# Kernel tuning notes

Hardware: AMD Instinct MI355X
Metric: run time of the kernel (lower is better)

## Reference

```python
import jax, jax.numpy as jnp
import numpy as np

WBITS_MAX = 3.0   # 3-bit signed narrow-range weights: levels in [-3, 3]
ABITS_MAX = 15.0  # 4-bit unsigned activations: levels in [0, 15]


def round_ste(x):
    # straight-through estimator for round (Brevitas uses STE)
    return x + jax.lax.stop_gradient(jnp.round(x) - x)


def quant_weight(w):
    # per-tensor symmetric narrow-range 3-bit fake quant (Int weight per-tensor float)
    s = jnp.max(jnp.abs(w)) / WBITS_MAX
    wq = jnp.clip(round_ste(w / s), -WBITS_MAX, WBITS_MAX) * s
    return wq, s


def quant_bias(b, w_scale, in_step):
    # Brevitas BiasQuant: bias scale = input_scale * weight_scale, no clipping (wide int)
    sb = w_scale * in_step  # in_step is shape (1,)
    return round_ste(b / sb) * sb


def quant_relu(x, s):
    # QuantReLU(bit_width=4): relu then unsigned 4-bit fake quant with learned scale s
    step = s / ABITS_MAX
    return jnp.clip(round_ste(jax.nn.relu(x) / step), 0.0, ABITS_MAX) * step


def conv2d(x, w):
    return jax.lax.conv_general_dilated(
        x, w, window_strides=(1, 1), padding='VALID',
        dimension_numbers=('NCHW', 'OIHW', 'NCHW'))


def maxpool2(x):
    return jax.lax.reduce_window(x, -jnp.inf, jax.lax.max,
                                 (1, 1, 2, 2), (1, 1, 2, 2), 'VALID')


def setup_inputs() -> dict:
    key = jax.random.key(0)
    ks = jax.random.split(key, 16)
    d = {}
    d['x'] = jax.random.normal(ks[0], (256, 3, 160, 160), jnp.float32)
    d['w1'] = jax.random.normal(ks[1], (6, 3, 3, 3), jnp.float32) * 0.2
    d['w2'] = jax.random.normal(ks[2], (12, 6, 3, 3), jnp.float32) * 0.2
    d['b2'] = jax.random.normal(ks[3], (12,), jnp.float32) * 0.1
    d['w3'] = jax.random.normal(ks[4], (18, 12, 3, 3), jnp.float32) * 0.2
    d['b3'] = jax.random.normal(ks[5], (18,), jnp.float32) * 0.1
    d['w4'] = jax.random.normal(ks[6], (18, 18, 3, 3), jnp.float32) * 0.2
    d['b4'] = jax.random.normal(ks[7], (18,), jnp.float32) * 0.1
    d['w5'] = jax.random.normal(ks[8], (18, 18, 3, 3), jnp.float32) * 0.2
    d['b5'] = jax.random.normal(ks[9], (18,), jnp.float32) * 0.1
    d['fw1'] = jax.random.normal(ks[10], (120, 162), jnp.float32) * 0.1
    d['fb1'] = jax.random.normal(ks[11], (120,), jnp.float32) * 0.1
    d['fw2'] = jax.random.normal(ks[12], (84, 120), jnp.float32) * 0.1
    d['fb2'] = jax.random.normal(ks[13], (84,), jnp.float32) * 0.1
    d['fw3'] = jax.random.normal(ks[14], (9, 84), jnp.float32) * 0.1
    for i in range(1, 8):
        d[f's{i}'] = jnp.full((1,), 6.0, jnp.float32)  # learned act scales (calibrated init)
    return d


def reference(x, w1, w2, b2, w3, b3, w4, b4, w5, b5,
              fw1, fb1, fw2, fb2, fw3, s1, s2, s3, s4, s5, s6, s7):
    # stage 1 (note: original forward feeds raw x into conv1, bypassing quant_inp)
    q1, _ = quant_weight(w1)
    out = maxpool2(quant_relu(conv2d(x, q1), s1))            # [B,6,79,79]
    # stage 2
    q2, ws2 = quant_weight(w2)
    bq2 = quant_bias(b2, ws2, s1 / ABITS_MAX)
    out = maxpool2(quant_relu(conv2d(out, q2) + bq2[None, :, None, None], s2))  # [B,12,38,38]
    # stage 3
    q3, ws3 = quant_weight(w3)
    bq3 = quant_bias(b3, ws3, s2 / ABITS_MAX)
    out = maxpool2(quant_relu(conv2d(out, q3) + bq3[None, :, None, None], s3))  # [B,18,18,18]
    # stage 4
    q4, ws4 = quant_weight(w4)
    bq4 = quant_bias(b4, ws4, s3 / ABITS_MAX)
    out = maxpool2(quant_relu(conv2d(out, q4) + bq4[None, :, None, None], s4))  # [B,18,8,8]
    # stage 5
    q5, ws5 = quant_weight(w5)
    bq5 = quant_bias(b5, ws5, s4 / ABITS_MAX)
    out = maxpool2(quant_relu(conv2d(out, q5) + bq5[None, :, None, None], s5))  # [B,18,3,3]
    out = out.reshape(out.shape[0], -1)                      # [B,162]
    # fc1
    qf1, fs1 = quant_weight(fw1)
    bqf1 = quant_bias(fb1, fs1, s5 / ABITS_MAX)
    out = quant_relu(out @ qf1.T + bqf1, s6)                 # [B,120]
    # fc2
    qf2, fs2 = quant_weight(fw2)
    bqf2 = quant_bias(fb2, fs2, s6 / ABITS_MAX)
    out = quant_relu(out @ qf2.T + bqf2, s7)                 # [B,84]
    # fc3 (no bias, output not re-quantized: return_quant_tensor=False default path)
    qf3, _ = quant_weight(fw3)
    return out @ qf3.T                                       # [B,9]
```

## Files before the change

### kernel.cpp

```cpp
#include <hip/hip_runtime.h>
#include <hip/hip_bf16.h>
#include <math.h>

constexpr size_t OFF_OUT1 = 0;
constexpr size_t OFF_OUT2 = (size_t)256 * 6 * 79 * 80;

template<int CIN, int COUT, int NCO, int HIN, int WSIN,
         int HPOOL, int WPOOL, int WSOUT, int XG, int RB,
         int THREADS, bool HAS_BIAS>
__global__ __launch_bounds__(THREADS)
void conv_stage(const float* __restrict__ in,
                const float* __restrict__ w_raw,
                const float* __restrict__ b_raw,
                const float* __restrict__ s_prev,
                const float* __restrict__ s_act,
                float* __restrict__ out)
{
    constexpr int GROUPS = COUT / NCO;
    constexpr int W4IN   = WSIN / 4;
    constexpr int NW     = COUT * CIN * 9;
    constexpr int STEPS  = 4 * CIN;
    static_assert(NCO * GROUPS == COUT, "NCO divides COUT");
    static_assert(GROUPS * XG * RB <= THREADS, "single compute pass");
    static_assert(4 * XG == WSOUT, "full padded row coverage");
    static_assert(WSIN % 4 == 0, "vec4 loads");

    __shared__ float lw[NW];
    __shared__ float lb[COUT];
    __shared__ float red[THREADS];

    const int r0  = blockIdx.x * RB;
    const int n   = blockIdx.y;
    const int tid = threadIdx.x;

    float mx = 0.0f;
    for (int i = tid; i < NW; i += THREADS) {
        const float v = w_raw[i];
        lw[i] = v;
        mx = fmaxf(mx, fabsf(v));
    }
    if (HAS_BIAS)
        for (int i = tid; i < COUT; i += THREADS) lb[i] = b_raw[i];
    red[tid] = mx;
    __syncthreads();
    for (int s = THREADS / 2; s > 0; s >>= 1) {
        if (tid < s) red[tid] = fmaxf(red[tid], red[tid + s]);
        __syncthreads();
    }
    const float sw_ = red[0] / 3.0f;
    for (int i = tid; i < NW; i += THREADS) {
        float q = rintf(lw[i] / sw_);
        q = fminf(fmaxf(q, -3.0f), 3.0f);
        lw[i] = q * sw_;
    }
    if (HAS_BIAS) {
        const float sb = sw_ * (s_prev[0] / 15.0f);
        for (int i = tid; i < COUT; i += THREADS)
            lb[i] = rintf(lb[i] / sb) * sb;
    }
    __syncthreads();

    const int o = tid;
    if (o >= GROUPS * XG * RB) return;
    const int cog = o % GROUPS;
    const int xg  = (o / GROUPS) % XG;
    const int ry  = o / (GROUPS * XG);
    const int r   = r0 + ry;
    if (r >= HPOOL) return;

    const float step = s_act[0] / 15.0f;

    const int u0 = 2 * xg;
    const int u1 = 2 * xg + 1;
    const int u2 = (2 * xg + 2 < W4IN) ? (2 * xg + 2) : (W4IN - 1);

    const float* base = in + (size_t)n * CIN * HIN * WSIN + (size_t)(2 * r) * WSIN;

    float acc[NCO][16];
#pragma unroll
    for (int j = 0; j < NCO; ++j)
#pragma unroll
        for (int i = 0; i < 16; ++i) acc[j][i] = 0.0f;

    float4 buf[3][3];
    float  wv[NCO][9];

#define ISSUE_STEP(S)                                                          \
    {                                                                          \
        const float* rp = base + (size_t)((S) >> 2) * HIN * WSIN               \
                               + (size_t)((S) & 3) * WSIN;                     \
        buf[(S) % 3][0] = *(const float4*)&rp[4 * u0];                         \
        buf[(S) % 3][1] = *(const float4*)&rp[4 * u1];                         \
        buf[(S) % 3][2] = *(const float4*)&rp[4 * u2];                         \
    }

    ISSUE_STEP(0);
    ISSUE_STEP(1);

#pragma unroll
    for (int s = 0; s < STEPS; ++s) {
        const int c  = s >> 2;
        const int rr = s & 3;

        if (s + 2 < STEPS) ISSUE_STEP(s + 2);

        if (rr == 0) {
#pragma unroll
            for (int j = 0; j < NCO; ++j)
#pragma unroll
                for (int k = 0; k < 9; ++k)
                    wv[j][k] = lw[((NCO * cog + j) * CIN + c) * 9 + k];
        }

        const float* row = (const float*)buf[s % 3];

        if (rr < 3) {
#pragma unroll
            for (int j = 0; j < NCO; ++j)
#pragma unroll
                for (int kc = 0; kc < 3; ++kc)
#pragma unroll
                    for (int xx = 0; xx < 8; ++xx)
                        acc[j][xx] = fmaf(row[xx + kc], wv[j][rr * 3 + kc], acc[j][xx]);
        }
        if (rr >= 1) {
#pragma unroll
            for (int j = 0; j < NCO; ++j)
#pragma unroll
                for (int kc = 0; kc < 3; ++kc)
#pragma unroll
                    for (int xx = 0; xx < 8; ++xx)
                        acc[j][8 + xx] = fmaf(row[xx + kc], wv[j][(rr - 1) * 3 + kc], acc[j][8 + xx]);
        }
    }
#undef ISSUE_STEP

#pragma unroll
    for (int j = 0; j < NCO; ++j) {
        const int co = NCO * cog + j;
        const float bias = HAS_BIAS ? lb[co] : 0.0f;
        float4 st;
#pragma unroll
        for (int t = 0; t < 4; ++t) {
            float m = fmaxf(fmaxf(acc[j][2 * t], acc[j][2 * t + 1]),
                            fmaxf(acc[j][8 + 2 * t], acc[j][8 + 2 * t + 1]));
            float v = fmaxf(m + bias, 0.0f);
            float q = rintf(v / step);
            q = fminf(fmaxf(q, 0.0f), 15.0f);
            ((float*)&st)[t] = (4 * xg + t < WPOOL) ? q * step : 0.0f;
        }
        *(float4*)&out[(((size_t)n * COUT + co) * HPOOL + r) * WSOUT + 4 * xg] = st;
    }
}

__global__ __launch_bounds__(512)
void tail_mega(const float* __restrict__ in2,
               const float* __restrict__ w3, const float* __restrict__ b3,
               const float* __restrict__ w4, const float* __restrict__ b4,
               const float* __restrict__ w5, const float* __restrict__ b5,
               const float* __restrict__ fw1, const float* __restrict__ fb1,
               const float* __restrict__ fw2, const float* __restrict__ fb2,
               const float* __restrict__ fw3,
               const float* __restrict__ s2, const float* __restrict__ s3,
               const float* __restrict__ s4, const float* __restrict__ s5,
               const float* __restrict__ s6, const float* __restrict__ s7,
               float* __restrict__ out)
{
    __shared__ float SL[12 * 38 * 40];
    __shared__ float A3[18 * 18 * 18];
    __shared__ float W3q[1944], W4q[2916], W5q[2916];
    __shared__ float B3q[18], B4q[18], B5q[18];
    __shared__ float O4[18 * 8 * 8];
    __shared__ float A5[162], A6[120], A7[84];

    const int n   = blockIdx.x;
    const int tid = threadIdx.x;
    float* red = A3;

    {
        const float4* src = (const float4*)(in2 + (size_t)n * 18240);
        float4* dst = (float4*)SL;
        for (int i = tid; i < 4560; i += 512) dst[i] = src[i];
    }
    float m3 = 0.f, m4 = 0.f, m5 = 0.f, g1 = 0.f, g2 = 0.f, g3 = 0.f;
    for (int i = tid; i < 1944; i += 512) { const float v = w3[i]; W3q[i] = v; m3 = fmaxf(m3, fabsf(v)); }
    for (int i = tid; i < 2916; i += 512) { const float v = w4[i]; W4q[i] = v; m4 = fmaxf(m4, fabsf(v)); }
    for (int i = tid; i < 2916; i += 512) { const float v = w5[i]; W5q[i] = v; m5 = fmaxf(m5, fabsf(v)); }
    for (int i = tid; i < 19440; i += 512) g1 = fmaxf(g1, fabsf(fw1[i]));
    for (int i = tid; i < 10080; i += 512) g2 = fmaxf(g2, fabsf(fw2[i]));
    for (int i = tid; i <   756; i += 512) g3 = fmaxf(g3, fabsf(fw3[i]));
    if (tid < 18) { B3q[tid] = b3[tid]; B4q[tid] = b4[tid]; B5q[tid] = b5[tid]; }
    red[0 * 512 + tid] = m3; red[1 * 512 + tid] = m4; red[2 * 512 + tid] = m5;
    red[3 * 512 + tid] = g1; red[4 * 512 + tid] = g2; red[5 * 512 + tid] = g3;
    __syncthreads();
    for (int s = 256; s > 0; s >>= 1) {
        if (tid < s)
#pragma unroll
            for (int j = 0; j < 6; ++j)
                red[j * 512 + tid] = fmaxf(red[j * 512 + tid], red[j * 512 + tid + s]);
        __syncthreads();
    }
    const float sw3 = red[0] / 3.0f, sw4 = red[512] / 3.0f, sw5 = red[1024] / 3.0f;
    const float sf1 = red[1536] / 3.0f, sf2 = red[2048] / 3.0f, sf3 = red[2560] / 3.0f;

    for (int i = tid; i < 1944; i += 512) { float q = rintf(W3q[i] / sw3); q = fminf(fmaxf(q, -3.f), 3.f); W3q[i] = q * sw3; }
    for (int i = tid; i < 2916; i += 512) { float q = rintf(W4q[i] / sw4); q = fminf(fmaxf(q, -3.f), 3.f); W4q[i] = q * sw4; }
    for (int i = tid; i < 2916; i += 512) { float q = rintf(W5q[i] / sw5); q = fminf(fmaxf(q, -3.f), 3.f); W5q[i] = q * sw5; }
    if (tid < 18) {
        const float sb3 = sw3 * (s2[0] / 15.0f); B3q[tid] = rintf(B3q[tid] / sb3) * sb3;
        const float sb4 = sw4 * (s3[0] / 15.0f); B4q[tid] = rintf(B4q[tid] / sb4) * sb4;
        const float sb5 = sw5 * (s4[0] / 15.0f); B5q[tid] = rintf(B5q[tid] / sb5) * sb5;
    }
    __syncthreads();

    {
        const float st = s3[0] / 15.0f;
        for (int it = tid; it < 972; it += 512) {
            const int r  = it / 54;
            const int rm = it - r * 54;
            const int co = rm / 3;
            const int th = rm - co * 3;

            float acc0[12], acc1[12];
#pragma unroll
            for (int i = 0; i < 12; ++i) { acc0[i] = 0.f; acc1[i] = 0.f; }

            for (int c = 0; c < 12; ++c) {
                float wv[9];
#pragma unroll
                for (int k = 0; k < 9; ++k) wv[k] = W3q[(co * 12 + c) * 9 + k];
#pragma unroll
                for (int rr = 0; rr < 4; ++rr) {
                    const float* rp = &SL[(c * 38 + 2 * r + rr) * 40 + 12 * th];
                    float row[14];
#pragma unroll
                    for (int v = 0; v < 7; ++v)
                        *(float2*)&row[2 * v] = *(const float2*)&rp[2 * v];
                    if (rr < 3) {
#pragma unroll
                        for (int kc = 0; kc < 3; ++kc)
#pragma unroll
                            for (int xx = 0; xx < 12; ++xx)
                                acc0[xx] = fmaf(row[xx + kc], wv[rr * 3 + kc], acc0[xx]);
                    }
                    if (rr >= 1) {
#pragma unroll
                        for (int kc = 0; kc < 3; ++kc)
#pragma unroll
                            for (int xx = 0; xx < 12; ++xx)
                                acc1[xx] = fmaf(row[xx + kc], wv[(rr - 1) * 3 + kc], acc1[xx]);
                    }
                }
            }
            const float bias = B3q[co];
#pragma unroll
            for (int x = 0; x < 6; ++x) {
                float m = fmaxf(fmaxf(acc0[2 * x], acc0[2 * x + 1]),
                                fmaxf(acc1[2 * x], acc1[2 * x + 1]));
                float v = fmaxf(m + bias, 0.0f);
                float q = rintf(v / st);
                q = fminf(fmaxf(q, 0.0f), 15.0f);
                A3[(co * 18 + r) * 18 + 6 * th + x] = q * st;
            }
        }
    }
    __syncthreads();

    {
        const float st = s4[0] / 15.0f;
        for (int o = tid; o < 1152; o += 512) {
            const int co = o >> 6;
            const int r  = (o >> 3) & 7;
            const int x  = o & 7;
            float a00 = 0.f, a01 = 0.f, a10 = 0.f, a11 = 0.f;
            for (int c = 0; c < 18; ++c) {
                float win[4][4];
#pragma unroll
                for (int rr = 0; rr < 4; ++rr) {
                    const int base = (c * 18 + 2 * r + rr) * 18 + 2 * x;
                    *(float2*)&win[rr][0] = *(const float2*)&A3[base];
                    *(float2*)&win[rr][2] = *(const float2*)&A3[base + 2];
                }
                const float* wp = &W4q[(co * 18 + c) * 9];
#pragma unroll
                for (int kr = 0; kr < 3; ++kr)
#pragma unroll
                    for (int kc = 0; kc < 3; ++kc) {
                        const float wv = wp[kr * 3 + kc];
                        a00 = fmaf(win[kr    ][kc    ], wv, a00);
                        a01 = fmaf(win[kr    ][kc + 1], wv, a01);
                        a10 = fmaf(win[kr + 1][kc    ], wv, a10);
                        a11 = fmaf(win[kr + 1][kc + 1], wv, a11);
                    }
            }
            float m = fmaxf(fmaxf(a00, a01), fmaxf(a10, a11));
            float v = fmaxf(m + B4q[co], 0.0f);
            float q = rintf(v / st);
            q = fminf(fmaxf(q, 0.0f), 15.0f);
            O4[o] = q * st;
        }
    }
    __syncthreads();

    {
        const float st = s5[0] / 15.0f;
        if (tid < 162) {
            const int co  = tid / 9;
            const int rem = tid - co * 9;
            const int r   = rem / 3;
            const int x   = rem - r * 3;
            float a00 = 0.f, a01 = 0.f, a10 = 0.f, a11 = 0.f;
            for (int c = 0; c < 18; ++c) {
                float win[4][4];
#pragma unroll
                for (int rr = 0; rr < 4; ++rr) {
                    const int base = c * 64 + (2 * r + rr) * 8 + 2 * x;
                    *(float2*)&win[rr][0] = *(const float2*)&O4[base];
                    *(float2*)&win[rr][2] = *(const float2*)&O4[base + 2];
                }
                const float* wp = &W5q[(co * 18 + c) * 9];
#pragma unroll
                for (int kr = 0; kr < 3; ++kr)
#pragma unroll
                    for (int kc = 0; kc < 3; ++kc) {
                        const float wv = wp[kr * 3 + kc];
                        a00 = fmaf(win[kr    ][kc    ], wv, a00);
                        a01 = fmaf(win[kr    ][kc + 1], wv, a01);
                        a10 = fmaf(win[kr + 1][kc    ], wv, a10);
                        a11 = fmaf(win[kr + 1][kc + 1], wv, a11);
                    }
            }
            float m = fmaxf(fmaxf(a00, a01), fmaxf(a10, a11));
            float v = fmaxf(m + B5q[co], 0.0f);
            float q = rintf(v / st);
            q = fminf(fmaxf(q, 0.0f), 15.0f);
            A5[tid] = q * st;
        }
    }
    __syncthreads();

    if (tid < 120) {
        float acc = 0.f;
        const float* wr = fw1 + (size_t)tid * 162;
#pragma unroll 6
        for (int k = 0; k < 162; ++k) {
            float q = rintf(wr[k] / sf1);
            q = fminf(fmaxf(q, -3.f), 3.f);
            acc = fmaf(A5[k], q * sf1, acc);
        }
        const float sb = sf1 * (s5[0] / 15.0f);
        acc += rintf(fb1[tid] / sb) * sb;
        const float st = s6[0] / 15.0f;
        float q = rintf(fmaxf(acc, 0.0f) / st);
        q = fminf(fmaxf(q, 0.0f), 15.0f);
        A6[tid] = q * st;
    }
    __syncthreads();

    if (tid < 84) {
        float acc = 0.f;
        const float* wr = fw2 + (size_t)tid * 120;
#pragma unroll 6
        for (int k = 0; k < 120; ++k) {
            float q = rintf(wr[k] / sf2);
            q = fminf(fmaxf(q, -3.f), 3.f);
            acc = fmaf(A6[k], q * sf2, acc);
        }
        const float sb = sf2 * (s6[0] / 15.0f);
        acc += rintf(fb2[tid] / sb) * sb;
        const float st = s7[0] / 15.0f;
        float q = rintf(fmaxf(acc, 0.0f) / st);
        q = fminf(fmaxf(q, 0.0f), 15.0f);
        A7[tid] = q * st;
    }
    __syncthreads();

    if (tid < 9) {
        float acc = 0.f;
        const float* wr = fw3 + (size_t)tid * 84;
#pragma unroll 6
        for (int k = 0; k < 84; ++k) {
            float q = rintf(wr[k] / sf3);
            q = fminf(fmaxf(q, -3.f), 3.f);
            acc = fmaf(A7[k], q * sf3, acc);
        }
        out[(size_t)n * 9 + tid] = acc;
    }
}

extern "C" void kernel_launch(void* const* d_in, const int* in_sizes, int n_in,
                              void* d_out, int out_size, void* d_ws, size_t ws_size,
                              hipStream_t stream)
{
    const float* x   = (const float*)d_in[0];
    const float* w1  = (const float*)d_in[1];
    const float* w2  = (const float*)d_in[2];
    const float* b2  = (const float*)d_in[3];
    const float* w3  = (const float*)d_in[4];
    const float* b3  = (const float*)d_in[5];
    const float* w4  = (const float*)d_in[6];
    const float* b4  = (const float*)d_in[7];
    const float* w5  = (const float*)d_in[8];
    const float* b5  = (const float*)d_in[9];
    const float* fw1 = (const float*)d_in[10];
    const float* fb1 = (const float*)d_in[11];
    const float* fw2 = (const float*)d_in[12];
    const float* fb2 = (const float*)d_in[13];
    const float* fw3 = (const float*)d_in[14];
    const float* s1  = (const float*)d_in[15];
    const float* s2  = (const float*)d_in[16];
    const float* s3  = (const float*)d_in[17];
    const float* s4  = (const float*)d_in[18];
    const float* s5  = (const float*)d_in[19];
    const float* s6  = (const float*)d_in[20];
    const float* s7  = (const float*)d_in[21];

    float* ws = (float*)d_ws;
    float* out = (float*)d_out;

    conv_stage<3, 6, 2, 160, 160, 79, 79, 80, 20, 4, 256, false>
        <<<dim3(20, 256), 256, 0, stream>>>(x, w1, nullptr, nullptr, s1, ws + OFF_OUT1);

    conv_stage<6, 12, 2, 79, 80, 38, 38, 40, 10, 4, 256, true>
        <<<dim3(10, 256), 256, 0, stream>>>(ws + OFF_OUT1, w2, b2, s1, s2, ws + OFF_OUT2);

    tail_mega<<<256, 512, 0, stream>>>(ws + OFF_OUT2,
                                       w3, b3, w4, b4, w5, b5,
                                       fw1, fb1, fw2, fb2, fw3,
                                       s2, s3, s4, s5, s6, s7, out);
}
```

Baseline: 152.8 us.

## Split conv3 out of tail megakernel into its own two-block-per-image stage

```diff
diff --git a/kernel.cpp b/kernel.cpp
--- a/kernel.cpp
+++ b/kernel.cpp
@@ -4,6 +4,7 @@
 
 constexpr size_t OFF_OUT1 = 0;
 constexpr size_t OFF_OUT2 = (size_t)256 * 6 * 79 * 80;
+constexpr size_t OFF_A3   = OFF_OUT1;
 
 template<int CIN, int COUT, int NCO, int HIN, int WSIN,
          int HPOOL, int WPOOL, int WSOUT, int XG, int RB,
@@ -154,115 +155,166 @@
 }
 
 __global__ __launch_bounds__(512)
-void tail_mega(const float* __restrict__ in2,
-               const float* __restrict__ w3, const float* __restrict__ b3,
-               const float* __restrict__ w4, const float* __restrict__ b4,
-               const float* __restrict__ w5, const float* __restrict__ b5,
-               const float* __restrict__ fw1, const float* __restrict__ fb1,
-               const float* __restrict__ fw2, const float* __restrict__ fb2,
-               const float* __restrict__ fw3,
-               const float* __restrict__ s2, const float* __restrict__ s3,
-               const float* __restrict__ s4, const float* __restrict__ s5,
-               const float* __restrict__ s6, const float* __restrict__ s7,
-               float* __restrict__ out)
+void conv3_stage(const float* __restrict__ in2,
+                 const float* __restrict__ w3, const float* __restrict__ b3,
+                 const float* __restrict__ s2, const float* __restrict__ s3,
+                 float* __restrict__ a3)
 {
-    __shared__ float SL[12 * 38 * 40];
-    __shared__ float A3[18 * 18 * 18];
-    __shared__ float W3q[1944], W4q[2916], W5q[2916];
-    __shared__ float B3q[18], B4q[18], B5q[18];
-    __shared__ float O4[18 * 8 * 8];
+    __shared__ float lw[1944];
+    __shared__ float lb[18];
+    __shared__ float red[512];
+
+    const int rb  = blockIdx.x;
+    const int n   = blockIdx.y;
+    const int tid = threadIdx.x;
+
+    float mx = 0.0f;
+    for (int i = tid; i < 1944; i += 512) {
+        const float v = w3[i];
+        lw[i] = v;
+        mx = fmaxf(mx, fabsf(v));
+    }
+    if (tid < 18) lb[tid] = b3[tid];
+    red[tid] = mx;
+    __syncthreads();
+    for (int s = 256; s > 0; s >>= 1) {
+        if (tid < s) red[tid] = fmaxf(red[tid], red[tid + s]);
+        __syncthreads();
+    }
+    const float sw = red[0] / 3.0f;
+    for (int i = tid; i < 1944; i += 512) {
+        float q = rintf(lw[i] / sw);
+        q = fminf(fmaxf(q, -3.0f), 3.0f);
+        lw[i] = q * sw;
+    }
+    if (tid < 18) {
+        const float sb = sw * (s2[0] / 15.0f);
+        lb[tid] = rintf(lb[tid] / sb) * sb;
+    }
+    __syncthreads();
+
+    if (tid >= 486) return;
+    const int rloc = tid / 54;
+    const int rm   = tid - rloc * 54;
+    const int co   = rm / 3;
+    const int th   = rm - co * 3;
+    const int r    = rb * 9 + rloc;
+
+    const float st = s3[0] / 15.0f;
+    const float* base = in2 + (size_t)n * 18240 + (size_t)(2 * r) * 40 + 12 * th;
+
+    float acc0[12], acc1[12];
+#pragma unroll
+    for (int i = 0; i < 12; ++i) { acc0[i] = 0.f; acc1[i] = 0.f; }
+
+    for (int c = 0; c < 12; ++c) {
+        float wv[9];
+#pragma unroll
+        for (int k = 0; k < 9; ++k) wv[k] = lw[(co * 12 + c) * 9 + k];
+        const float* cp = base + (size_t)c * 1520;
+#pragma unroll
+        for (int rr = 0; rr < 4; ++rr) {
+            const float* rp = cp + rr * 40;
+            float row[14];
+#pragma unroll
+            for (int v = 0; v < 7; ++v)
+                *(float2*)&row[2 * v] = *(const float2*)&rp[2 * v];
+            if (rr < 3) {
+#pragma unroll
+                for (int kc = 0; kc < 3; ++kc)
+#pragma unroll
+                    for (int xx = 0; xx < 12; ++xx)
+                        acc0[xx] = fmaf(row[xx + kc], wv[rr * 3 + kc], acc0[xx]);
+            }
+            if (rr >= 1) {
+#pragma unroll
+                for (int kc = 0; kc < 3; ++kc)
+#pragma unroll
+                    for (int xx = 0; xx < 12; ++xx)
+                        acc1[xx] = fmaf(row[xx + kc], wv[(rr - 1) * 3 + kc], acc1[xx]);
+            }
+        }
+    }
+
+    const float bias = lb[co];
+    float* orow = a3 + (size_t)n * 5832 + (size_t)co * 324 + (size_t)r * 18 + 6 * th;
+#pragma unroll
+    for (int x = 0; x < 6; ++x) {
+        float m = fmaxf(fmaxf(acc0[2 * x], acc0[2 * x + 1]),
+                        fmaxf(acc1[2 * x], acc1[2 * x + 1]));
+        float v = fmaxf(m + bias, 0.0f);
+        float q = rintf(v / st);
+        q = fminf(fmaxf(q, 0.0f), 15.0f);
+        orow[x] = q * st;
+    }
+}
+
+__global__ __launch_bounds__(512)
+void tail456(const float* __restrict__ a3in,
+             const float* __restrict__ w4, const float* __restrict__ b4,
+             const float* __restrict__ w5, const float* __restrict__ b5,
+             const float* __restrict__ fw1, const float* __restrict__ fb1,
+             const float* __restrict__ fw2, const float* __restrict__ fb2,
+             const float* __restrict__ fw3,
+             const float* __restrict__ s3, const float* __restrict__ s4,
+             const float* __restrict__ s5, const float* __restrict__ s6,
+             const float* __restrict__ s7,
+             float* __restrict__ out)
+{
+    __shared__ float A3[5832];
+    __shared__ float W4q[2916], W5q[2916];
+    __shared__ float B4q[18], B5q[18];
+    __shared__ float O4[1152];
     __shared__ float A5[162], A6[120], A7[84];
+    __shared__ float red[5 * 512];
 
     const int n   = blockIdx.x;
     const int tid = threadIdx.x;
-    float* red = A3;
 
     {
-        const float4* src = (const float4*)(in2 + (size_t)n * 18240);
-        float4* dst = (float4*)SL;
-        for (int i = tid; i < 4560; i += 512) dst[i] = src[i];
-    }
-    float m3 = 0.f, m4 = 0.f, m5 = 0.f, g1 = 0.f, g2 = 0.f, g3 = 0.f;
-    for (int i = tid; i < 1944; i += 512) { const float v = w3[i]; W3q[i] = v; m3 = fmaxf(m3, fabsf(v)); }
+        const float4* src = (const float4*)(a3in + (size_t)n * 5832);
+        float4* dst = (float4*)A3;
+        for (int i = tid; i < 1458; i += 512) dst[i] = src[i];
+    }
+    float m4 = 0.f, m5 = 0.f, g1 = 0.f, g2 = 0.f, g3 = 0.f;
     for (int i = tid; i < 2916; i += 512) { const float v = w4[i]; W4q[i] = v; m4 = fmaxf(m4, fabsf(v)); }
     for (int i = tid; i < 2916; i += 512) { const float v = w5[i]; W5q[i] = v; m5 = fmaxf(m5, fabsf(v)); }
-    for (int i = tid; i < 19440; i += 512) g1 = fmaxf(g1, fabsf(fw1[i]));
-    for (int i = tid; i < 10080; i += 512) g2 = fmaxf(g2, fabsf(fw2[i]));
-    for (int i = tid; i <   756; i += 512) g3 = fmaxf(g3, fabsf(fw3[i]));
-    if (tid < 18) { B3q[tid] = b3[tid]; B4q[tid] = b4[tid]; B5q[tid] = b5[tid]; }
-    red[0 * 512 + tid] = m3; red[1 * 512 + tid] = m4; red[2 * 512 + tid] = m5;
-    red[3 * 512 + tid] = g1; red[4 * 512 + tid] = g2; red[5 * 512 + tid] = g3;
+    {
+        const float4* f1 = (const float4*)fw1;
+        for (int i = tid; i < 4860; i += 512) {
+            const float4 v = f1[i];
+            g1 = fmaxf(g1, fmaxf(fmaxf(fabsf(v.x), fabsf(v.y)), fmaxf(fabsf(v.z), fabsf(v.w))));
+        }
+        const float4* f2 = (const float4*)fw2;
+        for (int i = tid; i < 2520; i += 512) {
+            const float4 v = f2[i];
+            g2 = fmaxf(g2, fmaxf(fmaxf(fabsf(v.x), fabsf(v.y)), fmaxf(fabsf(v.z), fabsf(v.w))));
+        }
+        const float4* f3 = (const float4*)fw3;
+        for (int i = tid; i < 189; i += 512) {
+            const float4 v = f3[i];
+            g3 = fmaxf(g3, fmaxf(fmaxf(fabsf(v.x), fabsf(v.y)), fmaxf(fabsf(v.z), fabsf(v.w))));
+        }
+    }
+    if (tid < 18) { B4q[tid] = b4[tid]; B5q[tid] = b5[tid]; }
+    red[tid] = m4; red[512 + tid] = m5; red[1024 + tid] = g1;
+    red[1536 + tid] = g2; red[2048 + tid] = g3;
     __syncthreads();
     for (int s = 256; s > 0; s >>= 1) {
         if (tid < s)
 #pragma unroll
-            for (int j = 0; j < 6; ++j)
+            for (int j = 0; j < 5; ++j)
                 red[j * 512 + tid] = fmaxf(red[j * 512 + tid], red[j * 512 + tid + s]);
         __syncthreads();
     }
-    const float sw3 = red[0] / 3.0f, sw4 = red[512] / 3.0f, sw5 = red[1024] / 3.0f;
-    const float sf1 = red[1536] / 3.0f, sf2 = red[2048] / 3.0f, sf3 = red[2560] / 3.0f;
-
-    for (int i = tid; i < 1944; i += 512) { float q = rintf(W3q[i] / sw3); q = fminf(fmaxf(q, -3.f), 3.f); W3q[i] = q * sw3; }
+    const float sw4 = red[0] / 3.0f, sw5 = red[512] / 3.0f;
+    const float sf1 = red[1024] / 3.0f, sf2 = red[1536] / 3.0f, sf3 = red[2048] / 3.0f;
+
     for (int i = tid; i < 2916; i += 512) { float q = rintf(W4q[i] / sw4); q = fminf(fmaxf(q, -3.f), 3.f); W4q[i] = q * sw4; }
     for (int i = tid; i < 2916; i += 512) { float q = rintf(W5q[i] / sw5); q = fminf(fmaxf(q, -3.f), 3.f); W5q[i] = q * sw5; }
     if (tid < 18) {
-        const float sb3 = sw3 * (s2[0] / 15.0f); B3q[tid] = rintf(B3q[tid] / sb3) * sb3;
         const float sb4 = sw4 * (s3[0] / 15.0f); B4q[tid] = rintf(B4q[tid] / sb4) * sb4;
         const float sb5 = sw5 * (s4[0] / 15.0f); B5q[tid] = rintf(B5q[tid] / sb5) * sb5;
-    }
-    __syncthreads();
-
-    {
-        const float st = s3[0] / 15.0f;
-        for (int it = tid; it < 972; it += 512) {
-            const int r  = it / 54;
-            const int rm = it - r * 54;
-            const int co = rm / 3;
-            const int th = rm - co * 3;
-
-            float acc0[12], acc1[12];
-#pragma unroll
-            for (int i = 0; i < 12; ++i) { acc0[i] = 0.f; acc1[i] = 0.f; }
-
-            for (int c = 0; c < 12; ++c) {
-                float wv[9];
-#pragma unroll
-                for (int k = 0; k < 9; ++k) wv[k] = W3q[(co * 12 + c) * 9 + k];
-#pragma unroll
-                for (int rr = 0; rr < 4; ++rr) {
-                    const float* rp = &SL[(c * 38 + 2 * r + rr) * 40 + 12 * th];
-                    float row[14];
-#pragma unroll
-                    for (int v = 0; v < 7; ++v)
-                        *(float2*)&row[2 * v] = *(const float2*)&rp[2 * v];
-                    if (rr < 3) {
-#pragma unroll
-                        for (int kc = 0; kc < 3; ++kc)
-#pragma unroll
-                            for (int xx = 0; xx < 12; ++xx)
-                                acc0[xx] = fmaf(row[xx + kc], wv[rr * 3 + kc], acc0[xx]);
-                    }
-                    if (rr >= 1) {
-#pragma unroll
-                        for (int kc = 0; kc < 3; ++kc)
-#pragma unroll
-                            for (int xx = 0; xx < 12; ++xx)
-                                acc1[xx] = fmaf(row[xx + kc], wv[(rr - 1) * 3 + kc], acc1[xx]);
-                    }
-                }
-            }
-            const float bias = B3q[co];
-#pragma unroll
-            for (int x = 0; x < 6; ++x) {
-                float m = fmaxf(fmaxf(acc0[2 * x], acc0[2 * x + 1]),
-                                fmaxf(acc1[2 * x], acc1[2 * x + 1]));
-                float v = fmaxf(m + bias, 0.0f);
-                float q = rintf(v / st);
-                q = fminf(fmaxf(q, 0.0f), 15.0f);
-                A3[(co * 18 + r) * 18 + 6 * th + x] = q * st;
-            }
-        }
     }
     __syncthreads();
 
@@ -277,7 +329,7 @@
                 float win[4][4];
 #pragma unroll
                 for (int rr = 0; rr < 4; ++rr) {
-                    const int base = (c * 18 + 2 * r + rr) * 18 + 2 * x;
+                    const int base = c * 324 + (2 * r + rr) * 18 + 2 * x;
                     *(float2*)&win[rr][0] = *(const float2*)&A3[base];
                     *(float2*)&win[rr][2] = *(const float2*)&A3[base + 2];
                 }
@@ -424,8 +476,10 @@
     conv_stage<6, 12, 2, 79, 80, 38, 38, 40, 10, 4, 256, true>
         <<<dim3(10, 256), 256, 0, stream>>>(ws + OFF_OUT1, w2, b2, s1, s2, ws + OFF_OUT2);
 
-    tail_mega<<<256, 512, 0, stream>>>(ws + OFF_OUT2,
-                                       w3, b3, w4, b4, w5, b5,
-                                       fw1, fb1, fw2, fb2, fw3,
-                                       s2, s3, s4, s5, s6, s7, out);
+    conv3_stage<<<dim3(2, 256), 512, 0, stream>>>(ws + OFF_OUT2, w3, b3, s2, s3, ws + OFF_A3);
+
+    tail456<<<256, 512, 0, stream>>>(ws + OFF_A3,
+                                     w4, b4, w5, b5,
+                                     fw1, fb1, fw2, fb2, fw3,
+                                     s3, s4, s5, s6, s7, out);
 }
```

Result: slower. 162.6 us (+6.4%).

## Store intermediate activations as uint8 quant levels and widen tail kernel

Applied to the files above, without the earlier changes.

```diff
diff --git a/kernel.cpp b/kernel.cpp
--- a/kernel.cpp
+++ b/kernel.cpp
@@ -1,21 +1,23 @@
 #include <hip/hip_runtime.h>
 #include <hip/hip_bf16.h>
 #include <math.h>
-
-constexpr size_t OFF_OUT1 = 0;
-constexpr size_t OFF_OUT2 = (size_t)256 * 6 * 79 * 80;
+#include <type_traits>
+
+constexpr size_t OFF_OUT1B = 0;
+constexpr size_t OFF_OUT2B = (size_t)256 * 6 * 79 * 80;
 
 template<int CIN, int COUT, int NCO, int HIN, int WSIN,
          int HPOOL, int WPOOL, int WSOUT, int XG, int RB,
-         int THREADS, bool HAS_BIAS>
+         int THREADS, bool HAS_BIAS, bool IN_U8>
 __global__ __launch_bounds__(THREADS)
-void conv_stage(const float* __restrict__ in,
+void conv_stage(const void* __restrict__ in_,
                 const float* __restrict__ w_raw,
                 const float* __restrict__ b_raw,
                 const float* __restrict__ s_prev,
                 const float* __restrict__ s_act,
-                float* __restrict__ out)
+                unsigned char* __restrict__ out)
 {
+    using TIN = typename std::conditional<IN_U8, unsigned char, float>::type;
     constexpr int GROUPS = COUT / NCO;
     constexpr int W4IN   = WSIN / 4;
     constexpr int NW     = COUT * CIN * 9;
@@ -69,12 +71,15 @@
     if (r >= HPOOL) return;
 
     const float step = s_act[0] / 15.0f;
+    float step_in = 0.0f;
+    if constexpr (IN_U8) step_in = s_prev[0] / 15.0f;
 
     const int u0 = 2 * xg;
     const int u1 = 2 * xg + 1;
     const int u2 = (2 * xg + 2 < W4IN) ? (2 * xg + 2) : (W4IN - 1);
 
-    const float* base = in + (size_t)n * CIN * HIN * WSIN + (size_t)(2 * r) * WSIN;
+    const TIN* in   = (const TIN*)in_;
+    const TIN* base = in + (size_t)n * CIN * HIN * WSIN + (size_t)(2 * r) * WSIN;
 
     float acc[NCO][16];
 #pragma unroll
@@ -82,16 +87,23 @@
 #pragma unroll
         for (int i = 0; i < 16; ++i) acc[j][i] = 0.0f;
 
-    float4 buf[3][3];
-    float  wv[NCO][9];
+    float4       fbuf[3][3];
+    unsigned int ubuf[3][3];
+    float        wv[NCO][9];
 
 #define ISSUE_STEP(S)                                                          \
     {                                                                          \
-        const float* rp = base + (size_t)((S) >> 2) * HIN * WSIN               \
-                               + (size_t)((S) & 3) * WSIN;                     \
-        buf[(S) % 3][0] = *(const float4*)&rp[4 * u0];                         \
-        buf[(S) % 3][1] = *(const float4*)&rp[4 * u1];                         \
-        buf[(S) % 3][2] = *(const float4*)&rp[4 * u2];                         \
+        const TIN* rp = base + (size_t)((S) >> 2) * HIN * WSIN                 \
+                             + (size_t)((S) & 3) * WSIN;                       \
+        if constexpr (IN_U8) {                                                 \
+            ubuf[(S) % 3][0] = *(const unsigned int*)&rp[4 * u0];              \
+            ubuf[(S) % 3][1] = *(const unsigned int*)&rp[4 * u1];              \
+            ubuf[(S) % 3][2] = *(const unsigned int*)&rp[4 * u2];              \
+        } else {                                                               \
+            fbuf[(S) % 3][0] = *(const float4*)&rp[4 * u0];                    \
+            fbuf[(S) % 3][1] = *(const float4*)&rp[4 * u1];                    \
+            fbuf[(S) % 3][2] = *(const float4*)&rp[4 * u2];                    \
+        }                                                                      \
     }
 
     ISSUE_STEP(0);
@@ -112,7 +124,20 @@
                     wv[j][k] = lw[((NCO * cog + j) * CIN + c) * 9 + k];
         }
 
-        const float* row = (const float*)buf[s % 3];
+        float row[12];
+        if constexpr (IN_U8) {
+#pragma unroll
+            for (int k = 0; k < 3; ++k) {
+                const unsigned int d = ubuf[s % 3][k];
+#pragma unroll
+                for (int b = 0; b < 4; ++b)
+                    row[4 * k + b] = (float)((d >> (8 * b)) & 0xffu) * step_in;
+            }
+        } else {
+            const float* rv = (const float*)fbuf[s % 3];
+#pragma unroll
+            for (int i = 0; i < 12; ++i) row[i] = rv[i];
+        }
 
         if (rr < 3) {
 #pragma unroll
@@ -139,7 +164,7 @@
     for (int j = 0; j < NCO; ++j) {
         const int co = NCO * cog + j;
         const float bias = HAS_BIAS ? lb[co] : 0.0f;
-        float4 st;
+        unsigned int pck = 0;
 #pragma unroll
         for (int t = 0; t < 4; ++t) {
             float m = fmaxf(fmaxf(acc[j][2 * t], acc[j][2 * t + 1]),
@@ -147,14 +172,22 @@
             float v = fmaxf(m + bias, 0.0f);
             float q = rintf(v / step);
             q = fminf(fmaxf(q, 0.0f), 15.0f);
-            ((float*)&st)[t] = (4 * xg + t < WPOOL) ? q * step : 0.0f;
-        }
-        *(float4*)&out[(((size_t)n * COUT + co) * HPOOL + r) * WSOUT + 4 * xg] = st;
+            const unsigned int qi = (4 * xg + t < WPOOL) ? (unsigned int)q : 0u;
+            pck |= qi << (8 * t);
+        }
+        *(unsigned int*)&out[(((size_t)n * COUT + co) * HPOOL + r) * WSOUT + 4 * xg] = pck;
     }
 }
 
-__global__ __launch_bounds__(512)
-void tail_mega(const float* __restrict__ in2,
+__device__ __forceinline__ float wave_max(float v) {
+#pragma unroll
+    for (int off = 32; off > 0; off >>= 1)
+        v = fmaxf(v, __shfl_down(v, off));
+    return v;
+}
+
+__global__ __launch_bounds__(1024)
+void tail_mega(const unsigned char* __restrict__ in2,
                const float* __restrict__ w3, const float* __restrict__ b3,
                const float* __restrict__ w4, const float* __restrict__ b4,
                const float* __restrict__ w5, const float* __restrict__ b5,
@@ -166,46 +199,67 @@
                const float* __restrict__ s6, const float* __restrict__ s7,
                float* __restrict__ out)
 {
-    __shared__ float SL[12 * 38 * 40];
-    __shared__ float A3[18 * 18 * 18];
+    __shared__ unsigned int SLu[4560];
+    __shared__ float A3[5832];
     __shared__ float W3q[1944], W4q[2916], W5q[2916];
     __shared__ float B3q[18], B4q[18], B5q[18];
-    __shared__ float O4[18 * 8 * 8];
+    __shared__ float O4[1152];
     __shared__ float A5[162], A6[120], A7[84];
-
-    const int n   = blockIdx.x;
-    const int tid = threadIdx.x;
-    float* red = A3;
+    __shared__ float sm[16][6];
+    __shared__ float scales[6];
+
+    const int n    = blockIdx.x;
+    const int tid  = threadIdx.x;
+    const int wid  = tid >> 6;
+    const int lane = tid & 63;
 
     {
-        const float4* src = (const float4*)(in2 + (size_t)n * 18240);
-        float4* dst = (float4*)SL;
-        for (int i = tid; i < 4560; i += 512) dst[i] = src[i];
+        const uint4* src = (const uint4*)(in2 + (size_t)n * 18240);
+        uint4* dst = (uint4*)SLu;
+        for (int i = tid; i < 1140; i += 1024) dst[i] = src[i];
     }
     float m3 = 0.f, m4 = 0.f, m5 = 0.f, g1 = 0.f, g2 = 0.f, g3 = 0.f;
-    for (int i = tid; i < 1944; i += 512) { const float v = w3[i]; W3q[i] = v; m3 = fmaxf(m3, fabsf(v)); }
-    for (int i = tid; i < 2916; i += 512) { const float v = w4[i]; W4q[i] = v; m4 = fmaxf(m4, fabsf(v)); }
-    for (int i = tid; i < 2916; i += 512) { const float v = w5[i]; W5q[i] = v; m5 = fmaxf(m5, fabsf(v)); }
-    for (int i = tid; i < 19440; i += 512) g1 = fmaxf(g1, fabsf(fw1[i]));
-    for (int i = tid; i < 10080; i += 512) g2 = fmaxf(g2, fabsf(fw2[i]));
-    for (int i = tid; i <   756; i += 512) g3 = fmaxf(g3, fabsf(fw3[i]));
+    for (int i = tid; i < 1944; i += 1024) { const float v = w3[i]; W3q[i] = v; m3 = fmaxf(m3, fabsf(v)); }
+    for (int i = tid; i < 2916; i += 1024) { const float v = w4[i]; W4q[i] = v; m4 = fmaxf(m4, fabsf(v)); }
+    for (int i = tid; i < 2916; i += 1024) { const float v = w5[i]; W5q[i] = v; m5 = fmaxf(m5, fabsf(v)); }
+    {
+        const float4* f1 = (const float4*)fw1;
+        for (int i = tid; i < 4860; i += 1024) {
+            const float4 v = f1[i];
+            g1 = fmaxf(g1, fmaxf(fmaxf(fabsf(v.x), fabsf(v.y)), fmaxf(fabsf(v.z), fabsf(v.w))));
+        }
+        const float4* f2 = (const float4*)fw2;
+        for (int i = tid; i < 2520; i += 1024) {
+            const float4 v = f2[i];
+            g2 = fmaxf(g2, fmaxf(fmaxf(fabsf(v.x), fabsf(v.y)), fmaxf(fabsf(v.z), fabsf(v.w))));
+        }
+        const float4* f3 = (const float4*)fw3;
+        for (int i = tid; i < 189; i += 1024) {
+            const float4 v = f3[i];
+            g3 = fmaxf(g3, fmaxf(fmaxf(fabsf(v.x), fabsf(v.y)), fmaxf(fabsf(v.z), fabsf(v.w))));
+        }
+    }
     if (tid < 18) { B3q[tid] = b3[tid]; B4q[tid] = b4[tid]; B5q[tid] = b5[tid]; }
-    red[0 * 512 + tid] = m3; red[1 * 512 + tid] = m4; red[2 * 512 + tid] = m5;
-    red[3 * 512 + tid] = g1; red[4 * 512 + tid] = g2; red[5 * 512 + tid] = g3;
-    __syncthreads();
-    for (int s = 256; s > 0; s >>= 1) {
-        if (tid < s)
-#pragma unroll
-            for (int j = 0; j < 6; ++j)
-                red[j * 512 + tid] = fmaxf(red[j * 512 + tid], red[j * 512 + tid + s]);
-        __syncthreads();
-    }
-    const float sw3 = red[0] / 3.0f, sw4 = red[512] / 3.0f, sw5 = red[1024] / 3.0f;
-    const float sf1 = red[1536] / 3.0f, sf2 = red[2048] / 3.0f, sf3 = red[2560] / 3.0f;
-
-    for (int i = tid; i < 1944; i += 512) { float q = rintf(W3q[i] / sw3); q = fminf(fmaxf(q, -3.f), 3.f); W3q[i] = q * sw3; }
-    for (int i = tid; i < 2916; i += 512) { float q = rintf(W4q[i] / sw4); q = fminf(fmaxf(q, -3.f), 3.f); W4q[i] = q * sw4; }
-    for (int i = tid; i < 2916; i += 512) { float q = rintf(W5q[i] / sw5); q = fminf(fmaxf(q, -3.f), 3.f); W5q[i] = q * sw5; }
+    m3 = wave_max(m3); m4 = wave_max(m4); m5 = wave_max(m5);
+    g1 = wave_max(g1); g2 = wave_max(g2); g3 = wave_max(g3);
+    if (lane == 0) {
+        sm[wid][0] = m3; sm[wid][1] = m4; sm[wid][2] = m5;
+        sm[wid][3] = g1; sm[wid][4] = g2; sm[wid][5] = g3;
+    }
+    __syncthreads();
+    if (tid < 6) {
+        float v = sm[0][tid];
+#pragma unroll
+        for (int w = 1; w < 16; ++w) v = fmaxf(v, sm[w][tid]);
+        scales[tid] = v / 3.0f;
+    }
+    __syncthreads();
+    const float sw3 = scales[0], sw4 = scales[1], sw5 = scales[2];
+    const float sf1 = scales[3], sf2 = scales[4], sf3 = scales[5];
+
+    for (int i = tid; i < 1944; i += 1024) { float q = rintf(W3q[i] / sw3); q = fminf(fmaxf(q, -3.f), 3.f); W3q[i] = q * sw3; }
+    for (int i = tid; i < 2916; i += 1024) { float q = rintf(W4q[i] / sw4); q = fminf(fmaxf(q, -3.f), 3.f); W4q[i] = q * sw4; }
+    for (int i = tid; i < 2916; i += 1024) { float q = rintf(W5q[i] / sw5); q = fminf(fmaxf(q, -3.f), 3.f); W5q[i] = q * sw5; }
     if (tid < 18) {
         const float sb3 = sw3 * (s2[0] / 15.0f); B3q[tid] = rintf(B3q[tid] / sb3) * sb3;
         const float sb4 = sw4 * (s3[0] / 15.0f); B4q[tid] = rintf(B4q[tid] / sb4) * sb4;
@@ -214,10 +268,12 @@
     __syncthreads();
 
     {
+        const unsigned char* SLb = (const unsigned char*)SLu;
+        const float step2 = s2[0] / 15.0f;
         const float st = s3[0] / 15.0f;
-        for (int it = tid; it < 972; it += 512) {
-            const int r  = it / 54;
-            const int rm = it - r * 54;
+        if (tid < 972) {
+            const int r  = tid / 54;
+            const int rm = tid - r * 54;
             const int co = rm / 3;
             const int th = rm - co * 3;
 
@@ -226,29 +282,33 @@
             for (int i = 0; i < 12; ++i) { acc0[i] = 0.f; acc1[i] = 0.f; }
 
             for (int c = 0; c < 12; ++c) {
-                float wv[9];
-#pragma unroll
-                for (int k = 0; k < 9; ++k) wv[k] = W3q[(co * 12 + c) * 9 + k];
+                float wvv[9];
+#pragma unroll
+                for (int k = 0; k < 9; ++k) wvv[k] = W3q[(co * 12 + c) * 9 + k];
 #pragma unroll
                 for (int rr = 0; rr < 4; ++rr) {
-                    const float* rp = &SL[(c * 38 + 2 * r + rr) * 40 + 12 * th];
-                    float row[14];
-#pragma unroll
-                    for (int v = 0; v < 7; ++v)
-                        *(float2*)&row[2 * v] = *(const float2*)&rp[2 * v];
+                    const int off = (c * 38 + 2 * r + rr) * 40 + 12 * th;
+                    float row[16];
+#pragma unroll
+                    for (int k = 0; k < 4; ++k) {
+                        const unsigned int d = *(const unsigned int*)&SLb[off + 4 * k];
+#pragma unroll
+                        for (int b = 0; b < 4; ++b)
+                            row[4 * k + b] = (float)((d >> (8 * b)) & 0xffu) * step2;
+                    }
                     if (rr < 3) {
 #pragma unroll
                         for (int kc = 0; kc < 3; ++kc)
 #pragma unroll
                             for (int xx = 0; xx < 12; ++xx)
-                                acc0[xx] = fmaf(row[xx + kc], wv[rr * 3 + kc], acc0[xx]);
+                                acc0[xx] = fmaf(row[xx + kc], wvv[rr * 3 + kc], acc0[xx]);
                     }
                     if (rr >= 1) {
 #pragma unroll
                         for (int kc = 0; kc < 3; ++kc)
 #pragma unroll
                             for (int xx = 0; xx < 12; ++xx)
-                                acc1[xx] = fmaf(row[xx + kc], wv[(rr - 1) * 3 + kc], acc1[xx]);
+                                acc1[xx] = fmaf(row[xx + kc], wvv[(rr - 1) * 3 + kc], acc1[xx]);
                     }
                 }
             }
@@ -268,7 +328,7 @@
 
     {
         const float st = s4[0] / 15.0f;
-        for (int o = tid; o < 1152; o += 512) {
+        for (int o = tid; o < 1152; o += 1024) {
             const int co = o >> 6;
             const int r  = (o >> 3) & 7;
             const int x  = o & 7;
@@ -277,7 +337,7 @@
                 float win[4][4];
 #pragma unroll
                 for (int rr = 0; rr < 4; ++rr) {
-                    const int base = (c * 18 + 2 * r + rr) * 18 + 2 * x;
+                    const int base = c * 324 + (2 * r + rr) * 18 + 2 * x;
                     *(float2*)&win[rr][0] = *(const float2*)&A3[base];
                     *(float2*)&win[rr][2] = *(const float2*)&A3[base + 2];
                 }
@@ -286,11 +346,11 @@
                 for (int kr = 0; kr < 3; ++kr)
 #pragma unroll
                     for (int kc = 0; kc < 3; ++kc) {
-                        const float wv = wp[kr * 3 + kc];
-                        a00 = fmaf(win[kr    ][kc    ], wv, a00);
-                        a01 = fmaf(win[kr    ][kc + 1], wv, a01);
-                        a10 = fmaf(win[kr + 1][kc    ], wv, a10);
-                        a11 = fmaf(win[kr + 1][kc + 1], wv, a11);
+                        const float wvv = wp[kr * 3 + kc];
+                        a00 = fmaf(win[kr    ][kc    ], wvv, a00);
+                        a01 = fmaf(win[kr    ][kc + 1], wvv, a01);
+                        a10 = fmaf(win[kr + 1][kc    ], wvv, a10);
+                        a11 = fmaf(win[kr + 1][kc + 1], wvv, a11);
                     }
             }
             float m = fmaxf(fmaxf(a00, a01), fmaxf(a10, a11));
@@ -323,11 +383,11 @@
                 for (int kr = 0; kr < 3; ++kr)
 #pragma unroll
                     for (int kc = 0; kc < 3; ++kc) {
-                        const float wv = wp[kr * 3 + kc];
-                        a00 = fmaf(win[kr    ][kc    ], wv, a00);
-                        a01 = fmaf(win[kr    ][kc + 1], wv, a01);
-                        a10 = fmaf(win[kr + 1][kc    ], wv, a10);
-                        a11 = fmaf(win[kr + 1][kc + 1], wv, a11);
+                        const float wvv = wp[kr * 3 + kc];
+                        a00 = fmaf(win[kr    ][kc    ], wvv, a00);
+                        a01 = fmaf(win[kr    ][kc + 1], wvv, a01);
+                        a10 = fmaf(win[kr + 1][kc    ], wvv, a10);
+                        a11 = fmaf(win[kr + 1][kc + 1], wvv, a11);
                     }
             }
             float m = fmaxf(fmaxf(a00, a01), fmaxf(a10, a11));
@@ -415,17 +475,19 @@
     const float* s6  = (const float*)d_in[20];
     const float* s7  = (const float*)d_in[21];
 
-    float* ws = (float*)d_ws;
+    unsigned char* wsb = (unsigned char*)d_ws;
     float* out = (float*)d_out;
 
-    conv_stage<3, 6, 2, 160, 160, 79, 79, 80, 20, 4, 256, false>
-        <<<dim3(20, 256), 256, 0, stream>>>(x, w1, nullptr, nullptr, s1, ws + OFF_OUT1);
-
-    conv_stage<6, 12, 2, 79, 80, 38, 38, 40, 10, 4, 256, true>
-        <<<dim3(10, 256), 256, 0, stream>>>(ws + OFF_OUT1, w2, b2, s1, s2, ws + OFF_OUT2);
-
-    tail_mega<<<256, 512, 0, stream>>>(ws + OFF_OUT2,
-                                       w3, b3, w4, b4, w5, b5,
-                                       fw1, fb1, fw2, fb2, fw3,
-                                       s2, s3, s4, s5, s6, s7, out);
+    conv_stage<3, 6, 2, 160, 160, 79, 79, 80, 20, 4, 256, false, false>
+        <<<dim3(20, 256), 256, 0, stream>>>(x, w1, nullptr, nullptr, s1,
+                                            wsb + OFF_OUT1B);
+
+    conv_stage<6, 12, 2, 79, 80, 38, 38, 40, 10, 4, 256, true, true>
+        <<<dim3(10, 256), 256, 0, stream>>>(wsb + OFF_OUT1B, w2, b2, s1, s2,
+                                            wsb + OFF_OUT2B);
+
+    tail_mega<<<256, 1024, 0, stream>>>(wsb + OFF_OUT2B,
+                                        w3, b3, w4, b4, w5, b5,
+                                        fw1, fb1, fw2, fb2, fw3,
+                                        s2, s3, s4, s5, s6, s7, out);
 }
```

Measured after the change: 138.9 us. -9.1%, faster.
